# Optimization experiments

Hardware: AMD Instinct MI355X
Metric: run time of the kernel (lower is better)

Reference implementation:

```python
import jax, jax.numpy as jnp
import numpy as np

N = 32768
E = 524288
B = 128
D = 256


def setup_inputs() -> dict:
    key = jax.random.key(0)
    ks = jax.random.split(key, 8)
    b_z = jax.random.normal(ks[0], (N, D), dtype=jnp.float32)
    src = jax.random.randint(ks[1], (E,), 0, N, dtype=jnp.int32)
    dst = jax.random.randint(ks[2], (E,), 0, N, dtype=jnp.int32)
    b_edge_weight = jax.random.uniform(ks[3], (E,), dtype=jnp.float32)
    # Glorot-ish init for layer weights (256->128->64->1)
    W1 = jax.random.normal(ks[4], (256, 128), dtype=jnp.float32) / np.sqrt(256)
    W2 = jax.random.normal(ks[5], (128, 64), dtype=jnp.float32) / np.sqrt(128)
    W3 = jax.random.normal(ks[6], (64, 1), dtype=jnp.float32) / np.sqrt(64)
    b1 = jnp.zeros((128,), jnp.float32)
    b2 = jnp.zeros((64,), jnp.float32)
    b3 = jnp.zeros((1,), jnp.float32)
    return {"b_z": b_z, "src": src, "dst": dst, "b_edge_weight": b_edge_weight,
            "W1": W1, "b1": b1, "W2": W2, "b2": b2, "W3": W3, "b3": b3,
            "b_size": B}


def _degree_norms(src, dst, n):
    ones = jnp.ones(src.shape[0], jnp.float32)
    out_deg = jax.ops.segment_sum(ones, src, num_segments=n)
    in_deg = jax.ops.segment_sum(ones, dst, num_segments=n)
    # DGL GraphConv norm='both': unweighted degrees, clamped to 1
    return jnp.clip(out_deg, 1.0) ** -0.5, jnp.clip(in_deg, 1.0) ** -0.5


def _gcn_layer(x, src, dst, ew, norm_src, norm_dst, W, b, use_tanh):
    # norm='both': scale source features, transform first (in_feats > out_feats),
    # weighted neighbor sum, then scale by in-degree norm, add bias, activate.
    h = (x * norm_src[:, None]) @ W            # [N, out]
    m = h[src] * ew[:, None]                   # [E, out] gathered messages
    agg = jax.ops.segment_sum(m, dst, num_segments=x.shape[0])  # [N, out]
    out = agg * norm_dst[:, None] + b
    return jnp.tanh(out) if use_tanh else out


def reference(b_z, src, dst, b_edge_weight, W1, b1, W2, b2, W3, b3, b_size):
    norm_src, norm_dst = _degree_norms(src, dst, b_z.shape[0])
    h = _gcn_layer(b_z, src, dst, b_edge_weight, norm_src, norm_dst, W1, b1, True)
    h = _gcn_layer(h, src, dst, b_edge_weight, norm_src, norm_dst, W2, b2, True)
    h = _gcn_layer(h, src, dst, b_edge_weight, norm_src, norm_dst, W3, b3, False)
    return h.reshape(b_size, -1)
```

## Files before the change

### kernel.cpp

```cpp
#include <hip/hip_runtime.h>


#define NB 256
#define NW4 8192
#define RSEG 8

typedef unsigned int uint32;
typedef unsigned char uchar_t;
typedef unsigned short ushort_t;
typedef __attribute__((ext_vector_type(8))) short bf16x8;
typedef __attribute__((ext_vector_type(4))) float f32x4;

__device__ inline ushort_t f2bf(float f) {
  uint32 u = __float_as_uint(f);
  u += 0x7fffu + ((u >> 16) & 1u);
  return (ushort_t)(u >> 16);
}
__device__ inline float bf2f(ushort_t h) { return __uint_as_float(((uint32)h) << 16); }

__global__ __launch_bounds__(1024) void lds_hist_kernel(const int* __restrict__ src,
                                                        const int* __restrict__ dst,
                                                        uint32* __restrict__ part,
                                                        int e, int epb) {
  __shared__ uint32 hs[NW4];
  __shared__ uint32 hd[NW4];
  const int t = threadIdx.x;
  for (int w = t; w < NW4; w += 1024) {
    hs[w] = 0;
    hd[w] = 0;
  }
  __syncthreads();
  const int base = blockIdx.x * epb;
  for (int k = t; k < epb; k += 1024) {
    int i = base + k;
    if (i < e) {
      int s = src[i], d = dst[i];
      atomicAdd(&hs[s >> 2], 1u << ((s & 3) * 8));
      atomicAdd(&hd[d >> 2], 1u << ((d & 3) * 8));
    }
  }
  __syncthreads();
  uint32* ps = part + (size_t)blockIdx.x * NW4;
  uint32* pd = part + (size_t)(NB + blockIdx.x) * NW4;
  for (int w = t; w < NW4; w += 1024) {
    ps[w] = hs[w];
    pd[w] = hd[w];
  }
}

__global__ __launch_bounds__(256) void norm_partial(const uint32* __restrict__ part,
                                                    uint32* __restrict__ psum, int n4) {
  const int w = blockIdx.x * 256 + threadIdx.x;
  const int seg = blockIdx.y;
  const int a = blockIdx.z;
  const uint32* p = part + (size_t)a * NB * n4 + (size_t)seg * (NB / RSEG) * n4 + w;
  uint32 s = 0;
#pragma unroll
  for (int r = 0; r < NB / RSEG; ++r) s += p[(size_t)r * n4];
  psum[(size_t)a * RSEG * n4 + (size_t)seg * n4 + w] = s;
}

__global__ __launch_bounds__(256) void norm_final(const uint32* __restrict__ psum,
                                                  float* __restrict__ norm_src,
                                                  float* __restrict__ norm_dst,
                                                  int* __restrict__ in_deg,
                                                  int* __restrict__ block_sums, int n4) {
  const int w = blockIdx.x * 256 + threadIdx.x;
  if (w >= n4) return;
  uint32 ss = 0, sd = 0;
#pragma unroll
  for (int seg = 0; seg < RSEG; ++seg) {
    ss += psum[(size_t)seg * n4 + w];
    sd += psum[(size_t)(RSEG + seg) * n4 + w];
  }
  int idsum = 0;
#pragma unroll
  for (int j = 0; j < 4; ++j) {
    int v = w * 4 + j;
    int od = (ss >> (j * 8)) & 0xff;
    int id = (sd >> (j * 8)) & 0xff;
    norm_src[v] = 1.0f / sqrtf((float)max(od, 1));
    norm_dst[v] = 1.0f / sqrtf((float)max(id, 1));
    in_deg[v] = id;
    idsum += id;
  }
#pragma unroll
  for (int off = 32; off > 0; off >>= 1) idsum += __shfl_down(idsum, off, 64);
  if ((threadIdx.x & 63) == 0) block_sums[w >> 6] = idsum;
}

__global__ __launch_bounds__(256) void scan_partials_b(int* __restrict__ block_sums,
                                                       int* __restrict__ block_offs, int nb) {
  __shared__ int sh[256];
  const int t = threadIdx.x;
  sh[t] = (t < nb) ? block_sums[t] : 0;
  __syncthreads();
  for (int off = 1; off < 256; off <<= 1) {
    int v = sh[t];
    int add = (t >= off) ? sh[t - off] : 0;
    __syncthreads();
    sh[t] = v + add;
    __syncthreads();
  }
  if (t < nb) block_offs[t] = (t > 0) ? sh[t - 1] : 0;
}

__global__ __launch_bounds__(256) void scan_write_goffs(const int* __restrict__ in_deg,
                                                        const int* __restrict__ block_offs,
                                                        const uint32* __restrict__ part_dst,
                                                        int* __restrict__ row_ptr,
                                                        uchar_t* __restrict__ gpre, int n) {
  __shared__ int sh[256];
  const int t = threadIdx.x;
  const int gid = blockIdx.x * 256 + t;
  int d = (gid < n) ? in_deg[gid] : 0;
  sh[t] = d;
  __syncthreads();
  for (int off = 1; off < 256; off <<= 1) {
    int v = sh[t];
    int add = (t >= off) ? sh[t - off] : 0;
    __syncthreads();
    sh[t] = v + add;
    __syncthreads();
  }
  if (gid >= n) return;
  int excl = block_offs[blockIdx.x] + sh[t] - d;
  row_ptr[gid] = excl;
  if (gid == n - 1) row_ptr[n] = excl + d;
  const int w = gid >> 2;
  const int shft = (gid & 3) * 8;
  const int n4 = n >> 2;
  int cum = 0;
#pragma unroll 8
  for (int r = 0; r < NB; ++r) {
    gpre[(size_t)r * n + gid] = (uchar_t)cum;
    cum += (part_dst[(size_t)r * n4 + w] >> shft) & 0xff;
  }
}

__global__ __launch_bounds__(1024) void scatter_kernel(const int* __restrict__ src,
                                                       const int* __restrict__ dst,
                                                       const float* __restrict__ ew,
                                                       const int* __restrict__ row_ptr,
                                                       const uchar_t* __restrict__ gpre,
                                                       int2* __restrict__ csr,
                                                       int n, int e, int epb) {
  __shared__ uint32 rk[NW4];
  const int t = threadIdx.x;
  for (int w = t; w < NW4; w += 1024) rk[w] = 0;
  __syncthreads();
  const int base = blockIdx.x * epb;
  const uchar_t* gp = gpre + (size_t)blockIdx.x * n;
  for (int k = t; k < epb; k += 1024) {
    int i = base + k;
    if (i < e) {
      int d = dst[i];
      uint32 sh = (d & 3) * 8;
      uint32 old = atomicAdd(&rk[d >> 2], 1u << sh);
      int rank = (old >> sh) & 0xff;
      int pos = row_ptr[d] + (int)gp[d] + rank;
      csr[pos] = make_int2(src[i], __float_as_int(ew[i]));
    }
  }
}

__global__ void wsplit_all(const float* __restrict__ W1, const float* __restrict__ W2,
                           ushort_t* __restrict__ WhT1, ushort_t* __restrict__ WlT1,
                           ushort_t* __restrict__ WhT2, ushort_t* __restrict__ WlT2) {
  int i = blockIdx.x * blockDim.x + threadIdx.x;
  if (i < 256 * 128) {
    int k = i / 128, c = i % 128;
    float f = W1[i];
    ushort_t h = f2bf(f);
    WhT1[(size_t)c * 256 + k] = h;
    WlT1[(size_t)c * 256 + k] = f2bf(f - bf2f(h));
  } else if (i < 256 * 128 + 128 * 64) {
    int j = i - 256 * 128;
    int k = j / 64, c = j % 64;
    float f = W2[j];
    ushort_t h = f2bf(f);
    WhT2[(size_t)c * 128 + k] = h;
    WlT2[(size_t)c * 128 + k] = f2bf(f - bf2f(h));
  }
}

template <int K, int OUT>
__global__ __launch_bounds__(256) void gemm_mfma(const float* __restrict__ x,
                                                 const ushort_t* __restrict__ WhT,
                                                 const ushort_t* __restrict__ WlT,
                                                 const float* __restrict__ norm_src,
                                                 ushort_t* __restrict__ ht, int n) {
  constexpr int BK = 64, KP = BK + 8;
  constexpr int NCT = OUT / 32;
  __shared__ ushort_t Xh[64][KP], Xl[64][KP];
  __shared__ ushort_t Wh[OUT][KP], Wl[OUT][KP];

  const int tid = threadIdx.x;
  const int wv = tid >> 6;
  const int lane = tid & 63;
  const int wr = wv >> 1;
  const int wc = wv & 1;
  const int row0 = blockIdx.x * 64;
  const int fr = lane & 15;
  const int fg = lane >> 4;

  f32x4 acc[2][NCT];
#pragma unroll
  for (int i = 0; i < 2; ++i)
#pragma unroll
    for (int j = 0; j < NCT; ++j) acc[i][j] = (f32x4){0.f, 0.f, 0.f, 0.f};

#pragma unroll 1
  for (int k0 = 0; k0 < K; k0 += BK) {
    __syncthreads();
#pragma unroll
    for (int p = 0; p < 4; ++p) {
      int idx = p * 256 + tid;
      int r = idx >> 4, c4 = idx & 15;
      float4 v = *reinterpret_cast<const float4*>(x + (size_t)(row0 + r) * K + k0 + c4 * 4);
      ushort4 h, l;
      h.x = f2bf(v.x); l.x = f2bf(v.x - bf2f(h.x));
      h.y = f2bf(v.y); l.y = f2bf(v.y - bf2f(h.y));
      h.z = f2bf(v.z); l.z = f2bf(v.z - bf2f(h.z));
      h.w = f2bf(v.w); l.w = f2bf(v.w - bf2f(h.w));
      *reinterpret_cast<ushort4*>(&Xh[r][c4 * 4]) = h;
      *reinterpret_cast<ushort4*>(&Xl[r][c4 * 4]) = l;
    }
#pragma unroll
    for (int p = 0; p < OUT * 16 / 256; ++p) {
      int idx = p * 256 + tid;
      int c = idx >> 4, k4 = idx & 15;
      *reinterpret_cast<ushort4*>(&Wh[c][k4 * 4]) =
          *reinterpret_cast<const ushort4*>(WhT + (size_t)c * K + k0 + k4 * 4);
      *reinterpret_cast<ushort4*>(&Wl[c][k4 * 4]) =
          *reinterpret_cast<const ushort4*>(WlT + (size_t)c * K + k0 + k4 * 4);
    }
    __syncthreads();

#pragma unroll
    for (int s = 0; s < 2; ++s) {
      const int kk = s * 32 + fg * 8;
      bf16x8 ah[2], al[2];
#pragma unroll
      for (int i = 0; i < 2; ++i) {
        int r = wr * 32 + i * 16 + fr;
        ah[i] = *reinterpret_cast<const bf16x8*>(&Xh[r][kk]);
        al[i] = *reinterpret_cast<const bf16x8*>(&Xl[r][kk]);
      }
#pragma unroll
      for (int j = 0; j < NCT; ++j) {
        int c = wc * (OUT / 2) + j * 16 + fr;
        bf16x8 bh = *reinterpret_cast<const bf16x8*>(&Wh[c][kk]);
        bf16x8 bl = *reinterpret_cast<const bf16x8*>(&Wl[c][kk]);
#pragma unroll
        for (int i = 0; i < 2; ++i) {
          acc[i][j] = __builtin_amdgcn_mfma_f32_16x16x32_bf16(ah[i], bh, acc[i][j], 0, 0, 0);
          acc[i][j] = __builtin_amdgcn_mfma_f32_16x16x32_bf16(ah[i], bl, acc[i][j], 0, 0, 0);
          acc[i][j] = __builtin_amdgcn_mfma_f32_16x16x32_bf16(al[i], bh, acc[i][j], 0, 0, 0);
        }
      }
    }
  }

#pragma unroll
  for (int i = 0; i < 2; ++i) {
#pragma unroll
    for (int q = 0; q < 4; ++q) {
      int row = row0 + wr * 32 + i * 16 + fg * 4 + q;
      float ns = norm_src[row];
#pragma unroll
      for (int j = 0; j < NCT; ++j) {
        int col = wc * (OUT / 2) + j * 16 + fr;
        ht[(size_t)row * OUT + col] = f2bf(acc[i][j][q] * ns);
      }
    }
  }
}

#define GATHB(e, acc)                                                               \
  {                                                                                 \
    float w_ = __int_as_float(e.y);                                                 \
    ushort4 h_ = *reinterpret_cast<const ushort4*>(ht + (size_t)e.x * OUT + cg * 4);\
    acc.x += w_ * bf2f(h_.x);                                                       \
    acc.y += w_ * bf2f(h_.y);                                                       \
    acc.z += w_ * bf2f(h_.z);                                                       \
    acc.w += w_ * bf2f(h_.w);                                                       \
  }

template <int OUT>
__global__ void aggregate_kernel(const ushort_t* __restrict__ ht, const int* __restrict__ row_ptr,
                                 const int2* __restrict__ csr, const float* __restrict__ norm_dst,
                                 const float* __restrict__ bias, float* __restrict__ out, int n) {
  constexpr int LPN = OUT / 4;
  constexpr int NPB = 256 / LPN;
  const int tid = threadIdx.x;
  const int cg = tid % LPN;
  const int v = blockIdx.x * NPB + tid / LPN;
  if (v >= n) return;

  const int s0 = row_ptr[v];
  const int s1 = row_ptr[v + 1];
  float4 a0 = {0, 0, 0, 0}, a1 = {0, 0, 0, 0}, a2 = {0, 0, 0, 0}, a3 = {0, 0, 0, 0};
  int i = s0;
  for (; i + 4 <= s1; i += 4) {
    int2 e0 = csr[i], e1 = csr[i + 1], e2 = csr[i + 2], e3 = csr[i + 3];
    GATHB(e0, a0);
    GATHB(e1, a1);
    GATHB(e2, a2);
    GATHB(e3, a3);
  }
  for (; i < s1; ++i) {
    int2 e = csr[i];
    GATHB(e, a0);
  }
  float nd = norm_dst[v];
  float4 b4 = *reinterpret_cast<const float4*>(bias + cg * 4);
  float4 r;
  r.x = tanhf((a0.x + a1.x + a2.x + a3.x) * nd + b4.x);
  r.y = tanhf((a0.y + a1.y + a2.y + a3.y) * nd + b4.y);
  r.z = tanhf((a0.z + a1.z + a2.z + a3.z) * nd + b4.z);
  r.w = tanhf((a0.w + a1.w + a2.w + a3.w) * nd + b4.w);
  *reinterpret_cast<float4*>(out + (size_t)v * OUT + cg * 4) = r;
}

__global__ void aggregate2_fuse3(const ushort_t* __restrict__ ht, const int* __restrict__ row_ptr,
                                 const int2* __restrict__ csr, const float* __restrict__ norm_dst,
                                 const float* __restrict__ norm_src, const float* __restrict__ bias,
                                 const float* __restrict__ W3, float* __restrict__ ht3, int n) {
  constexpr int OUT = 64;
  constexpr int LPN = OUT / 4;
  constexpr int NPB = 256 / LPN;
  const int tid = threadIdx.x;
  const int cg = tid % LPN;
  const int v = blockIdx.x * NPB + tid / LPN;
  if (v >= n) return;

  const int s0 = row_ptr[v];
  const int s1 = row_ptr[v + 1];
  float4 a0 = {0, 0, 0, 0}, a1 = {0, 0, 0, 0}, a2 = {0, 0, 0, 0}, a3 = {0, 0, 0, 0};
  int i = s0;
  for (; i + 4 <= s1; i += 4) {
    int2 e0 = csr[i], e1 = csr[i + 1], e2 = csr[i + 2], e3 = csr[i + 3];
    GATHB(e0, a0);
    GATHB(e1, a1);
    GATHB(e2, a2);
    GATHB(e3, a3);
  }
  for (; i < s1; ++i) {
    int2 e = csr[i];
    GATHB(e, a0);
  }
  float nd = norm_dst[v];
  float4 b4 = *reinterpret_cast<const float4*>(bias + cg * 4);
  float ox = tanhf((a0.x + a1.x + a2.x + a3.x) * nd + b4.x);
  float oy = tanhf((a0.y + a1.y + a2.y + a3.y) * nd + b4.y);
  float oz = tanhf((a0.z + a1.z + a2.z + a3.z) * nd + b4.z);
  float ow = tanhf((a0.w + a1.w + a2.w + a3.w) * nd + b4.w);
  float4 w3 = *reinterpret_cast<const float4*>(W3 + cg * 4);
  float p = ox * w3.x + oy * w3.y + oz * w3.z + ow * w3.w;
#pragma unroll
  for (int m = 1; m < 16; m <<= 1) p += __shfl_xor(p, m, 64);
  if (cg == 0) ht3[v] = p * norm_src[v];
}

__global__ void aggregate3_kernel(const float* __restrict__ ht3, const int* __restrict__ row_ptr,
                                  const int2* __restrict__ csr, const float* __restrict__ norm_dst,
                                  const float* __restrict__ b3, float* __restrict__ out, int n) {
  int v = blockIdx.x * blockDim.x + threadIdx.x;
  if (v >= n) return;
  const int s0 = row_ptr[v];
  const int s1 = row_ptr[v + 1];
  float p0 = 0.f, p1 = 0.f, p2 = 0.f, p3 = 0.f;
  int i = s0;
  for (; i + 4 <= s1; i += 4) {
    int2 e0 = csr[i], e1 = csr[i + 1], e2 = csr[i + 2], e3 = csr[i + 3];
    p0 += __int_as_float(e0.y) * ht3[e0.x];
    p1 += __int_as_float(e1.y) * ht3[e1.x];
    p2 += __int_as_float(e2.y) * ht3[e2.x];
    p3 += __int_as_float(e3.y) * ht3[e3.x];
  }
  for (; i < s1; ++i) {
    int2 e = csr[i];
    p0 += __int_as_float(e.y) * ht3[e.x];
  }
  out[v] = (p0 + p1 + p2 + p3) * norm_dst[v] + b3[0];
}

extern "C" void kernel_launch(void* const* d_in, const int* in_sizes, int n_in,
                              void* d_out, int out_size, void* d_ws, size_t ws_size,
                              hipStream_t stream) {
  const float* b_z = (const float*)d_in[0];
  const int* src = (const int*)d_in[1];
  const int* dst = (const int*)d_in[2];
  const float* ew = (const float*)d_in[3];
  const float* W1 = (const float*)d_in[4];
  const float* b1 = (const float*)d_in[5];
  const float* W2 = (const float*)d_in[6];
  const float* b2 = (const float*)d_in[7];
  const float* W3 = (const float*)d_in[8];
  const float* b3 = (const float*)d_in[9];

  const int N = in_sizes[0] / 256;
  const int E = in_sizes[1];
  const int N4 = N / 4;
  const int epb = (E + NB - 1) / NB;

  char* ws = (char*)d_ws;
  size_t off = 0;
  auto alloc = [&](size_t bytes) -> void* {
    void* p = ws + off;
    off += (bytes + 255) & ~(size_t)255;
    return p;
  };

  uint32* part = (uint32*)alloc((size_t)2 * NB * N4 * 4);
  uint32* psum = (uint32*)alloc((size_t)2 * RSEG * N4 * 4);
  uchar_t* gpre = (uchar_t*)alloc((size_t)NB * N);
  float* norm_src = (float*)alloc((size_t)N * 4);
  float* norm_dst = (float*)alloc((size_t)N * 4);
  int* in_deg = (int*)alloc((size_t)N * 4);
  int* row_ptr = (int*)alloc((size_t)(N + 1) * 4);
  int* block_sums = (int*)alloc(256 * 4);
  int* block_offs = (int*)alloc(256 * 4);
  int2* csr = (int2*)alloc((size_t)E * 8);
  ushort_t* HT = (ushort_t*)alloc((size_t)N * 128 * 2);
  float* ACT1 = (float*)alloc((size_t)N * 128 * 4);
  float* HT3 = (float*)alloc((size_t)N * 4);
  ushort_t* WhT1 = (ushort_t*)alloc((size_t)256 * 128 * 2);
  ushort_t* WlT1 = (ushort_t*)alloc((size_t)256 * 128 * 2);
  ushort_t* WhT2 = (ushort_t*)alloc((size_t)128 * 64 * 2);
  ushort_t* WlT2 = (ushort_t*)alloc((size_t)128 * 64 * 2);

  const uint32* part_dst = part + (size_t)NB * N4;
  const int nBlocks = (N + 255) / 256;

  lds_hist_kernel<<<NB, 1024, 0, stream>>>(src, dst, part, E, epb);
  norm_partial<<<dim3(N4 / 256, RSEG, 2), 256, 0, stream>>>(part, psum, N4);
  norm_final<<<N4 / 256, 256, 0, stream>>>(psum, norm_src, norm_dst, in_deg, block_sums, N4);
  scan_partials_b<<<1, 256, 0, stream>>>(block_sums, block_offs, nBlocks);
  scan_write_goffs<<<nBlocks, 256, 0, stream>>>(in_deg, block_offs, part_dst, row_ptr, gpre, N);
  scatter_kernel<<<NB, 1024, 0, stream>>>(src, dst, ew, row_ptr, gpre, csr, N, E, epb);
  wsplit_all<<<(256 * 128 + 128 * 64 + 255) / 256, 256, 0, stream>>>(W1, W2, WhT1, WlT1,
                                                                     WhT2, WlT2);

  gemm_mfma<256, 128><<<N / 64, 256, 0, stream>>>(b_z, WhT1, WlT1, norm_src, HT, N);
  aggregate_kernel<128><<<(N + 7) / 8, 256, 0, stream>>>(HT, row_ptr, csr, norm_dst, b1, ACT1, N);
  gemm_mfma<128, 64><<<N / 64, 256, 0, stream>>>(ACT1, WhT2, WlT2, norm_src, HT, N);
  aggregate2_fuse3<<<(N + 15) / 16, 256, 0, stream>>>(HT, row_ptr, csr, norm_dst, norm_src, b2,
                                                      W3, HT3, N);
  aggregate3_kernel<<<nBlocks, 256, 0, stream>>>(HT3, row_ptr, csr, norm_dst, b3,
                                                 (float*)d_out, N);
}
```

Measured before the change: 111.5 us.

## Fuse weight split into histogram, fold norm_src into edges, bf16 layer-1 activations

```diff
diff --git a/kernel.cpp b/kernel.cpp
--- a/kernel.cpp
+++ b/kernel.cpp
@@ -18,13 +18,32 @@
 }
 __device__ inline float bf2f(ushort_t h) { return __uint_as_float(((uint32)h) << 16); }
 
-__global__ __launch_bounds__(1024) void lds_hist_kernel(const int* __restrict__ src,
-                                                        const int* __restrict__ dst,
-                                                        uint32* __restrict__ part,
-                                                        int e, int epb) {
+__global__ __launch_bounds__(1024) void hist_wsplit_kernel(
+    const int* __restrict__ src, const int* __restrict__ dst, uint32* __restrict__ part,
+    const float* __restrict__ W1, const float* __restrict__ W2,
+    ushort_t* __restrict__ WhT1, ushort_t* __restrict__ WlT1,
+    ushort_t* __restrict__ WhT2, ushort_t* __restrict__ WlT2, int e, int epb) {
+  const int t = threadIdx.x;
+  if (blockIdx.x >= NB) {
+    int i = (blockIdx.x - NB) * 1024 + t;
+    if (i < 256 * 128) {
+      int k = i / 128, c = i % 128;
+      float f = W1[i];
+      ushort_t h = f2bf(f);
+      WhT1[(size_t)c * 256 + k] = h;
+      WlT1[(size_t)c * 256 + k] = f2bf(f - bf2f(h));
+    } else if (i < 256 * 128 + 128 * 64) {
+      int j = i - 256 * 128;
+      int k = j / 64, c = j % 64;
+      float f = W2[j];
+      ushort_t h = f2bf(f);
+      WhT2[(size_t)c * 128 + k] = h;
+      WlT2[(size_t)c * 128 + k] = f2bf(f - bf2f(h));
+    }
+    return;
+  }
   __shared__ uint32 hs[NW4];
   __shared__ uint32 hd[NW4];
-  const int t = threadIdx.x;
   for (int w = t; w < NW4; w += 1024) {
     hs[w] = 0;
     hd[w] = 0;
@@ -89,30 +108,24 @@
   if ((threadIdx.x & 63) == 0) block_sums[w >> 6] = idsum;
 }
 
-__global__ __launch_bounds__(256) void scan_partials_b(int* __restrict__ block_sums,
-                                                       int* __restrict__ block_offs, int nb) {
-  __shared__ int sh[256];
-  const int t = threadIdx.x;
-  sh[t] = (t < nb) ? block_sums[t] : 0;
-  __syncthreads();
-  for (int off = 1; off < 256; off <<= 1) {
-    int v = sh[t];
-    int add = (t >= off) ? sh[t - off] : 0;
-    __syncthreads();
-    sh[t] = v + add;
-    __syncthreads();
-  }
-  if (t < nb) block_offs[t] = (t > 0) ? sh[t - 1] : 0;
-}
-
 __global__ __launch_bounds__(256) void scan_write_goffs(const int* __restrict__ in_deg,
-                                                        const int* __restrict__ block_offs,
+                                                        const int* __restrict__ block_sums,
                                                         const uint32* __restrict__ part_dst,
                                                         int* __restrict__ row_ptr,
                                                         uchar_t* __restrict__ gpre, int n) {
   __shared__ int sh[256];
+  __shared__ int s_boff;
   const int t = threadIdx.x;
   const int gid = blockIdx.x * 256 + t;
+  {
+    int v = (t < blockIdx.x && t < 128) ? block_sums[t] : 0;
+#pragma unroll
+    for (int off = 32; off > 0; off >>= 1) v += __shfl_down(v, off, 64);
+    if ((t & 63) == 0) sh[t >> 6] = v;
+    __syncthreads();
+    if (t == 0) s_boff = sh[0] + sh[1] + sh[2] + sh[3];
+    __syncthreads();
+  }
   int d = (gid < n) ? in_deg[gid] : 0;
   sh[t] = d;
   __syncthreads();
@@ -124,7 +137,7 @@
     __syncthreads();
   }
   if (gid >= n) return;
-  int excl = block_offs[blockIdx.x] + sh[t] - d;
+  int excl = s_boff + sh[t] - d;
   row_ptr[gid] = excl;
   if (gid == n - 1) row_ptr[n] = excl + d;
   const int w = gid >> 2;
@@ -141,6 +154,7 @@
 __global__ __launch_bounds__(1024) void scatter_kernel(const int* __restrict__ src,
                                                        const int* __restrict__ dst,
                                                        const float* __restrict__ ew,
+                                                       const float* __restrict__ norm_src,
                                                        const int* __restrict__ row_ptr,
                                                        const uchar_t* __restrict__ gpre,
                                                        int2* __restrict__ csr,
@@ -154,33 +168,14 @@
   for (int k = t; k < epb; k += 1024) {
     int i = base + k;
     if (i < e) {
+      int s = src[i];
       int d = dst[i];
       uint32 sh = (d & 3) * 8;
       uint32 old = atomicAdd(&rk[d >> 2], 1u << sh);
       int rank = (old >> sh) & 0xff;
       int pos = row_ptr[d] + (int)gp[d] + rank;
-      csr[pos] = make_int2(src[i], __float_as_int(ew[i]));
-    }
-  }
-}
-
-__global__ void wsplit_all(const float* __restrict__ W1, const float* __restrict__ W2,
-                           ushort_t* __restrict__ WhT1, ushort_t* __restrict__ WlT1,
-                           ushort_t* __restrict__ WhT2, ushort_t* __restrict__ WlT2) {
-  int i = blockIdx.x * blockDim.x + threadIdx.x;
-  if (i < 256 * 128) {
-    int k = i / 128, c = i % 128;
-    float f = W1[i];
-    ushort_t h = f2bf(f);
-    WhT1[(size_t)c * 256 + k] = h;
-    WlT1[(size_t)c * 256 + k] = f2bf(f - bf2f(h));
-  } else if (i < 256 * 128 + 128 * 64) {
-    int j = i - 256 * 128;
-    int k = j / 64, c = j % 64;
-    float f = W2[j];
-    ushort_t h = f2bf(f);
-    WhT2[(size_t)c * 128 + k] = h;
-    WlT2[(size_t)c * 128 + k] = f2bf(f - bf2f(h));
+      csr[pos] = make_int2(s, __float_as_int(ew[i] * norm_src[s]));
+    }
   }
 }
 
@@ -188,10 +183,10 @@
 __global__ __launch_bounds__(256) void gemm_mfma(const float* __restrict__ x,
                                                  const ushort_t* __restrict__ WhT,
                                                  const ushort_t* __restrict__ WlT,
-                                                 const float* __restrict__ norm_src,
                                                  ushort_t* __restrict__ ht, int n) {
   constexpr int BK = 64, KP = BK + 8;
   constexpr int NCT = OUT / 32;
+  constexpr int NWLD = OUT * 16 / 256;
   __shared__ ushort_t Xh[64][KP], Xl[64][KP];
   __shared__ ushort_t Wh[OUT][KP], Wl[OUT][KP];
 
@@ -210,6 +205,30 @@
 #pragma unroll
     for (int j = 0; j < NCT; ++j) acc[i][j] = (f32x4){0.f, 0.f, 0.f, 0.f};
 
+  float4 xr[4];
+  ushort4 wrh[NWLD], wrl[NWLD];
+
+#define LOADX(kg)                                                                       \
+  {                                                                                     \
+    _Pragma("unroll") for (int p_ = 0; p_ < 4; ++p_) {                                  \
+      int idx_ = p_ * 256 + tid;                                                        \
+      xr[p_] = *reinterpret_cast<const float4*>(                                        \
+          x + (size_t)(row0 + (idx_ >> 4)) * K + (kg) + (idx_ & 15) * 4);               \
+    }                                                                                   \
+  }
+#define LOADW(kg)                                                                       \
+  {                                                                                     \
+    _Pragma("unroll") for (int p_ = 0; p_ < NWLD; ++p_) {                               \
+      int idx_ = p_ * 256 + tid;                                                        \
+      int c_ = idx_ >> 4, k4_ = idx_ & 15;                                              \
+      wrh[p_] = *reinterpret_cast<const ushort4*>(WhT + (size_t)c_ * K + (kg) + k4_ * 4);\
+      wrl[p_] = *reinterpret_cast<const ushort4*>(WlT + (size_t)c_ * K + (kg) + k4_ * 4);\
+    }                                                                                   \
+  }
+
+  LOADX(0);
+  LOADW(0);
+
 #pragma unroll 1
   for (int k0 = 0; k0 < K; k0 += BK) {
     __syncthreads();
@@ -217,7 +236,7 @@
     for (int p = 0; p < 4; ++p) {
       int idx = p * 256 + tid;
       int r = idx >> 4, c4 = idx & 15;
-      float4 v = *reinterpret_cast<const float4*>(x + (size_t)(row0 + r) * K + k0 + c4 * 4);
+      float4 v = xr[p];
       ushort4 h, l;
       h.x = f2bf(v.x); l.x = f2bf(v.x - bf2f(h.x));
       h.y = f2bf(v.y); l.y = f2bf(v.y - bf2f(h.y));
@@ -227,13 +246,15 @@
       *reinterpret_cast<ushort4*>(&Xl[r][c4 * 4]) = l;
     }
 #pragma unroll
-    for (int p = 0; p < OUT * 16 / 256; ++p) {
+    for (int p = 0; p < NWLD; ++p) {
       int idx = p * 256 + tid;
       int c = idx >> 4, k4 = idx & 15;
-      *reinterpret_cast<ushort4*>(&Wh[c][k4 * 4]) =
-          *reinterpret_cast<const ushort4*>(WhT + (size_t)c * K + k0 + k4 * 4);
-      *reinterpret_cast<ushort4*>(&Wl[c][k4 * 4]) =
-          *reinterpret_cast<const ushort4*>(WlT + (size_t)c * K + k0 + k4 * 4);
+      *reinterpret_cast<ushort4*>(&Wh[c][k4 * 4]) = wrh[p];
+      *reinterpret_cast<ushort4*>(&Wl[c][k4 * 4]) = wrl[p];
+    }
+    if (k0 + BK < K) {
+      LOADX(k0 + BK);
+      LOADW(k0 + BK);
     }
     __syncthreads();
 
@@ -261,17 +282,126 @@
       }
     }
   }
+#undef LOADX
+#undef LOADW
 
 #pragma unroll
   for (int i = 0; i < 2; ++i) {
 #pragma unroll
     for (int q = 0; q < 4; ++q) {
       int row = row0 + wr * 32 + i * 16 + fg * 4 + q;
-      float ns = norm_src[row];
 #pragma unroll
       for (int j = 0; j < NCT; ++j) {
         int col = wc * (OUT / 2) + j * 16 + fr;
-        ht[(size_t)row * OUT + col] = f2bf(acc[i][j][q] * ns);
+        ht[(size_t)row * OUT + col] = f2bf(acc[i][j][q]);
+      }
+    }
+  }
+}
+
+template <int K, int OUT>
+__global__ __launch_bounds__(256) void gemm_mfma_bf16in(const ushort_t* __restrict__ x,
+                                                        const ushort_t* __restrict__ WhT,
+                                                        const ushort_t* __restrict__ WlT,
+                                                        ushort_t* __restrict__ ht, int n) {
+  constexpr int BK = 64, KP = BK + 8;
+  constexpr int NCT = OUT / 32;
+  constexpr int NWLD = OUT * 16 / 256;
+  __shared__ ushort_t Xh[64][KP];
+  __shared__ ushort_t Wh[OUT][KP], Wl[OUT][KP];
+
+  const int tid = threadIdx.x;
+  const int wv = tid >> 6;
+  const int lane = tid & 63;
+  const int wr = wv >> 1;
+  const int wc = wv & 1;
+  const int row0 = blockIdx.x * 64;
+  const int fr = lane & 15;
+  const int fg = lane >> 4;
+
+  f32x4 acc[2][NCT];
+#pragma unroll
+  for (int i = 0; i < 2; ++i)
+#pragma unroll
+    for (int j = 0; j < NCT; ++j) acc[i][j] = (f32x4){0.f, 0.f, 0.f, 0.f};
+
+  ushort4 xr[4];
+  ushort4 wrh[NWLD], wrl[NWLD];
+
+#define LOADX(kg)                                                                       \
+  {                                                                                     \
+    _Pragma("unroll") for (int p_ = 0; p_ < 4; ++p_) {                                  \
+      int idx_ = p_ * 256 + tid;                                                        \
+      xr[p_] = *reinterpret_cast<const ushort4*>(                                       \
+          x + (size_t)(row0 + (idx_ >> 4)) * K + (kg) + (idx_ & 15) * 4);               \
+    }                                                                                   \
+  }
+#define LOADW(kg)                                                                       \
+  {                                                                                     \
+    _Pragma("unroll") for (int p_ = 0; p_ < NWLD; ++p_) {                               \
+      int idx_ = p_ * 256 + tid;                                                        \
+      int c_ = idx_ >> 4, k4_ = idx_ & 15;                                              \
+      wrh[p_] = *reinterpret_cast<const ushort4*>(WhT + (size_t)c_ * K + (kg) + k4_ * 4);\
+      wrl[p_] = *reinterpret_cast<const ushort4*>(WlT + (size_t)c_ * K + (kg) + k4_ * 4);\
+    }                                                                                   \
+  }
+
+  LOADX(0);
+  LOADW(0);
+
+#pragma unroll 1
+  for (int k0 = 0; k0 < K; k0 += BK) {
+    __syncthreads();
+#pragma unroll
+    for (int p = 0; p < 4; ++p) {
+      int idx = p * 256 + tid;
+      *reinterpret_cast<ushort4*>(&Xh[idx >> 4][(idx & 15) * 4]) = xr[p];
+    }
+#pragma unroll
+    for (int p = 0; p < NWLD; ++p) {
+      int idx = p * 256 + tid;
+      int c = idx >> 4, k4 = idx & 15;
+      *reinterpret_cast<ushort4*>(&Wh[c][k4 * 4]) = wrh[p];
+      *reinterpret_cast<ushort4*>(&Wl[c][k4 * 4]) = wrl[p];
+    }
+    if (k0 + BK < K) {
+      LOADX(k0 + BK);
+      LOADW(k0 + BK);
+    }
+    __syncthreads();
+
+#pragma unroll
+    for (int s = 0; s < 2; ++s) {
+      const int kk = s * 32 + fg * 8;
+      bf16x8 ah[2];
+#pragma unroll
+      for (int i = 0; i < 2; ++i)
+        ah[i] = *reinterpret_cast<const bf16x8*>(&Xh[wr * 32 + i * 16 + fr][kk]);
+#pragma unroll
+      for (int j = 0; j < NCT; ++j) {
+        int c = wc * (OUT / 2) + j * 16 + fr;
+        bf16x8 bh = *reinterpret_cast<const bf16x8*>(&Wh[c][kk]);
+        bf16x8 bl = *reinterpret_cast<const bf16x8*>(&Wl[c][kk]);
+#pragma unroll
+        for (int i = 0; i < 2; ++i) {
+          acc[i][j] = __builtin_amdgcn_mfma_f32_16x16x32_bf16(ah[i], bh, acc[i][j], 0, 0, 0);
+          acc[i][j] = __builtin_amdgcn_mfma_f32_16x16x32_bf16(ah[i], bl, acc[i][j], 0, 0, 0);
+        }
+      }
+    }
+  }
+#undef LOADX
+#undef LOADW
+
+#pragma unroll
+  for (int i = 0; i < 2; ++i) {
+#pragma unroll
+    for (int q = 0; q < 4; ++q) {
+      int row = row0 + wr * 32 + i * 16 + fg * 4 + q;
+#pragma unroll
+      for (int j = 0; j < NCT; ++j) {
+        int col = wc * (OUT / 2) + j * 16 + fr;
+        ht[(size_t)row * OUT + col] = f2bf(acc[i][j][q]);
       }
     }
   }
@@ -290,7 +420,8 @@
 template <int OUT>
 __global__ void aggregate_kernel(const ushort_t* __restrict__ ht, const int* __restrict__ row_ptr,
                                  const int2* __restrict__ csr, const float* __restrict__ norm_dst,
-                                 const float* __restrict__ bias, float* __restrict__ out, int n) {
+                                 const float* __restrict__ bias, ushort_t* __restrict__ out,
+                                 int n) {
   constexpr int LPN = OUT / 4;
   constexpr int NPB = 256 / LPN;
   const int tid = threadIdx.x;
@@ -315,18 +446,18 @@
   }
   float nd = norm_dst[v];
   float4 b4 = *reinterpret_cast<const float4*>(bias + cg * 4);
-  float4 r;
-  r.x = tanhf((a0.x + a1.x + a2.x + a3.x) * nd + b4.x);
-  r.y = tanhf((a0.y + a1.y + a2.y + a3.y) * nd + b4.y);
-  r.z = tanhf((a0.z + a1.z + a2.z + a3.z) * nd + b4.z);
-  r.w = tanhf((a0.w + a1.w + a2.w + a3.w) * nd + b4.w);
-  *reinterpret_cast<float4*>(out + (size_t)v * OUT + cg * 4) = r;
+  ushort4 r;
+  r.x = f2bf(tanhf((a0.x + a1.x + a2.x + a3.x) * nd + b4.x));
+  r.y = f2bf(tanhf((a0.y + a1.y + a2.y + a3.y) * nd + b4.y));
+  r.z = f2bf(tanhf((a0.z + a1.z + a2.z + a3.z) * nd + b4.z));
+  r.w = f2bf(tanhf((a0.w + a1.w + a2.w + a3.w) * nd + b4.w));
+  *reinterpret_cast<ushort4*>(out + (size_t)v * OUT + cg * 4) = r;
 }
 
 __global__ void aggregate2_fuse3(const ushort_t* __restrict__ ht, const int* __restrict__ row_ptr,
                                  const int2* __restrict__ csr, const float* __restrict__ norm_dst,
-                                 const float* __restrict__ norm_src, const float* __restrict__ bias,
-                                 const float* __restrict__ W3, float* __restrict__ ht3, int n) {
+                                 const float* __restrict__ bias, const float* __restrict__ W3,
+                                 float* __restrict__ ht3, int n) {
   constexpr int OUT = 64;
   constexpr int LPN = OUT / 4;
   constexpr int NPB = 256 / LPN;
@@ -360,7 +491,7 @@
   float p = ox * w3.x + oy * w3.y + oz * w3.z + ow * w3.w;
 #pragma unroll
   for (int m = 1; m < 16; m <<= 1) p += __shfl_xor(p, m, 64);
-  if (cg == 0) ht3[v] = p * norm_src[v];
+  if (cg == 0) ht3[v] = p;
 }
 
 __global__ void aggregate3_kernel(const float* __restrict__ ht3, const int* __restrict__ row_ptr,
@@ -421,10 +552,9 @@
   int* in_deg = (int*)alloc((size_t)N * 4);
   int* row_ptr = (int*)alloc((size_t)(N + 1) * 4);
   int* block_sums = (int*)alloc(256 * 4);
-  int* block_offs = (int*)alloc(256 * 4);
   int2* csr = (int2*)alloc((size_t)E * 8);
   ushort_t* HT = (ushort_t*)alloc((size_t)N * 128 * 2);
-  float* ACT1 = (float*)alloc((size_t)N * 128 * 4);
+  ushort_t* ACT1 = (ushort_t*)alloc((size_t)N * 128 * 2);
   float* HT3 = (float*)alloc((size_t)N * 4);
   ushort_t* WhT1 = (ushort_t*)alloc((size_t)256 * 128 * 2);
   ushort_t* WlT1 = (ushort_t*)alloc((size_t)256 * 128 * 2);
@@ -433,21 +563,19 @@
 
   const uint32* part_dst = part + (size_t)NB * N4;
   const int nBlocks = (N + 255) / 256;
-
-  lds_hist_kernel<<<NB, 1024, 0, stream>>>(src, dst, part, E, epb);
+  const int wsBlocks = (256 * 128 + 128 * 64 + 1023) / 1024;
+
+  hist_wsplit_kernel<<<NB + wsBlocks, 1024, 0, stream>>>(src, dst, part, W1, W2, WhT1, WlT1,
+                                                         WhT2, WlT2, E, epb);
   norm_partial<<<dim3(N4 / 256, RSEG, 2), 256, 0, stream>>>(part, psum, N4);
   norm_final<<<N4 / 256, 256, 0, stream>>>(psum, norm_src, norm_dst, in_deg, block_sums, N4);
-  scan_partials_b<<<1, 256, 0, stream>>>(block_sums, block_offs, nBlocks);
-  scan_write_goffs<<<nBlocks, 256, 0, stream>>>(in_deg, block_offs, part_dst, row_ptr, gpre, N);
-  scatter_kernel<<<NB, 1024, 0, stream>>>(src, dst, ew, row_ptr, gpre, csr, N, E, epb);
-  wsplit_all<<<(256 * 128 + 128 * 64 + 255) / 256, 256, 0, stream>>>(W1, W2, WhT1, WlT1,
-                                                                     WhT2, WlT2);
-
-  gemm_mfma<256, 128><<<N / 64, 256, 0, stream>>>(b_z, WhT1, WlT1, norm_src, HT, N);
+  scan_write_goffs<<<nBlocks, 256, 0, stream>>>(in_deg, block_sums, part_dst, row_ptr, gpre, N);
+  scatter_kernel<<<NB, 1024, 0, stream>>>(src, dst, ew, norm_src, row_ptr, gpre, csr, N, E, epb);
+
+  gemm_mfma<256, 128><<<N / 64, 256, 0, stream>>>(b_z, WhT1, WlT1, HT, N);
   aggregate_kernel<128><<<(N + 7) / 8, 256, 0, stream>>>(HT, row_ptr, csr, norm_dst, b1, ACT1, N);
-  gemm_mfma<128, 64><<<N / 64, 256, 0, stream>>>(ACT1, WhT2, WlT2, norm_src, HT, N);
-  aggregate2_fuse3<<<(N + 15) / 16, 256, 0, stream>>>(HT, row_ptr, csr, norm_dst, norm_src, b2,
-                                                      W3, HT3, N);
+  gemm_mfma_bf16in<128, 64><<<N / 64, 256, 0, stream>>>(ACT1, WhT2, WlT2, HT, N);
+  aggregate2_fuse3<<<(N + 15) / 16, 256, 0, stream>>>(HT, row_ptr, csr, norm_dst, b2, W3, HT3, N);
   aggregate3_kernel<<<nBlocks, 256, 0, stream>>>(HT3, row_ptr, csr, norm_dst, b3,
                                                  (float*)d_out, N);
 }
```

New measurement: 107.7 us. 1.03x faster.
